# Kernel optimization log

Measured on AMD Instinct MI355X. Metric: run time of the kernel, lower is better.

The kernel has to match this reference:

```python
import jax, jax.numpy as jnp
import numpy as np

T, B, D, H = 1024, 8, 1024, 16

def setup_inputs() -> dict:
    key = jax.random.key(0)
    ks = jax.random.split(key, 9)
    s = 0.02
    return {
        "x": jax.random.normal(ks[0], (T, B, D), dtype=jnp.float32),
        "Wq": jax.random.normal(ks[1], (D, D), dtype=jnp.float32) * s,
        "bq": jnp.zeros((D,), dtype=jnp.float32),
        "Wk": jax.random.normal(ks[2], (D, D), dtype=jnp.float32) * s,
        "bk": jnp.zeros((D,), dtype=jnp.float32),
        "Wv": jax.random.normal(ks[3], (D, D), dtype=jnp.float32) * s,
        "bv": jnp.zeros((D,), dtype=jnp.float32),
        "Wo": jax.random.normal(ks[4], (D, D), dtype=jnp.float32) * s,
        "bo": jnp.zeros((D,), dtype=jnp.float32),
        "n_heads": H,
    }

def reference(x, Wq, bq, Wk, bk, Wv, bv, Wo, bo, n_heads):
    t, b, D = x.shape
    h = n_heads
    d = D // h
    scale = 1.0 / jnp.sqrt(jnp.float32(d))
    # nn.Linear: y = x @ W.T + b
    q = (x @ Wq.T + bq).reshape(t, b, h, d)
    k = (x @ Wk.T + bk).reshape(t, b, h, d)
    v = (x @ Wv.T + bv).reshape(t, b, h, d)
    # scores: [b, h, t_query, t_key]
    scores = jnp.einsum('tbhd,sbhd->bhts', q, k) * scale
    attn = jax.nn.softmax(scores, axis=-1)
    out = jnp.einsum('bhts,sbhd->tbhd', attn, v).reshape(t, b, D)
    return out @ Wo.T + bo
```

## Files before the change

### kernel.cpp

```cpp
#include <hip/hip_runtime.h>


#define Tn 1024
#define Bn 8
#define Dn 1024
#define Hn 16
#define HDn 64
#define Mn 8192
#define Kn 1024

typedef float f32x4 __attribute__((ext_vector_type(4)));
typedef __bf16 bf16x8 __attribute__((ext_vector_type(8)));
typedef unsigned short u16x8 __attribute__((ext_vector_type(8)));
typedef unsigned short u16x4 __attribute__((ext_vector_type(4)));

#define GLL16(g, l)                                                        \
  __builtin_amdgcn_global_load_lds(                                        \
      (const __attribute__((address_space(1))) void*)(g),                  \
      (__attribute__((address_space(3))) void*)(l), 16, 0, 0)

__device__ __forceinline__ unsigned short f2bf(float f) {
  unsigned int u = __float_as_uint(f);
  u += 0x7fffu + ((u >> 16) & 1u);
  return (unsigned short)(u >> 16);
}

__device__ __forceinline__ unsigned short bfbits(float f) {
  __bf16 h = (__bf16)f;
  return __builtin_bit_cast(unsigned short, h);
}

__global__ __launch_bounds__(256) void cvt_all(
    const float* __restrict__ x, const float* __restrict__ w0,
    const float* __restrict__ w1, const float* __restrict__ w2,
    const float* __restrict__ w3, unsigned short* __restrict__ dx,
    unsigned short* __restrict__ d0, unsigned short* __restrict__ d1,
    unsigned short* __restrict__ d2, unsigned short* __restrict__ d3) {
  const int NX = Mn * Kn / 4;
  const int NW = Dn * Dn / 4;
  const int NT = NX + 4 * NW;
  int i = blockIdx.x * 256 + threadIdx.x;
  const int stride = gridDim.x * 256;
  for (; i < NT; i += stride) {
    const float* src;
    unsigned short* dst;
    int j;
    if (i < NX) {
      src = x; dst = dx; j = i;
    } else {
      const int t = i - NX;
      const int wsel = t >> 18;
      j = t & (NW - 1);
      src = (wsel == 0) ? w0 : (wsel == 1) ? w1 : (wsel == 2) ? w2 : w3;
      dst = (wsel == 0) ? d0 : (wsel == 1) ? d1 : (wsel == 2) ? d2 : d3;
    }
    const float4 v = ((const float4*)src)[j];
    u16x4 o;
    o.x = f2bf(v.x); o.y = f2bf(v.y); o.z = f2bf(v.z); o.w = f2bf(v.w);
    ((u16x4*)dst)[j] = o;
  }
}

__device__ __forceinline__ void gemm128_core(
    const unsigned short* __restrict__ A, const unsigned short* __restrict__ Bw,
    unsigned short* lds_a, unsigned short* lds_b,
    int bm, int bn, f32x4 acc[4][4]) {
  const int tid = threadIdx.x;
  const int lane = tid & 63;
  const int w = tid >> 6;
  const int wr = w >> 1, wc = w & 1;
  const int fr = lane & 15, fg = lane >> 4;

  int goffA[4], goffB[4];
#pragma unroll
  for (int i = 0; i < 4; i++) {
    const int p = tid + 256 * i;
    const int r = p >> 3, cblk = (p & 7) ^ (r & 7);
    goffA[i] = (bm * 128 + r) * Kn + cblk * 8;
    goffB[i] = (bn * 128 + r) * Kn + cblk * 8;
  }
  int aoff[4][2], boff[4][2];
#pragma unroll
  for (int m = 0; m < 4; m++) {
    const int row = wr * 64 + m * 16 + fr;
#pragma unroll
    for (int kk = 0; kk < 2; kk++)
      aoff[m][kk] = row * 64 + (((kk * 4 + fg) ^ (row & 7)) * 8);
  }
#pragma unroll
  for (int n = 0; n < 4; n++) {
    const int row = wc * 64 + n * 16 + fr;
#pragma unroll
    for (int kk = 0; kk < 2; kk++)
      boff[n][kk] = row * 64 + (((kk * 4 + fg) ^ (row & 7)) * 8);
  }

  for (int kt = 0; kt < 16; ++kt) {
    const int kbase = kt * 64;
#pragma unroll
    for (int i = 0; i < 4; i++) {
      GLL16(A + goffA[i] + kbase, &lds_a[(tid + 256 * i) * 8]);
      GLL16(Bw + goffB[i] + kbase, &lds_b[(tid + 256 * i) * 8]);
    }
    __syncthreads();
#pragma unroll
    for (int kk = 0; kk < 2; kk++) {
      bf16x8 af[4], bfr[4];
#pragma unroll
      for (int m = 0; m < 4; m++) af[m] = *(const bf16x8*)&lds_a[aoff[m][kk]];
#pragma unroll
      for (int n = 0; n < 4; n++) bfr[n] = *(const bf16x8*)&lds_b[boff[n][kk]];
#pragma unroll
      for (int m = 0; m < 4; m++)
#pragma unroll
        for (int n = 0; n < 4; n++)
          acc[m][n] = __builtin_amdgcn_mfma_f32_16x16x32_bf16(
              af[m], bfr[n], acc[m][n], 0, 0, 0);
    }
    __syncthreads();
  }
}

__global__ __launch_bounds__(256) void gemm_qkv(
    const unsigned short* __restrict__ xbf, const unsigned short* __restrict__ wq,
    const unsigned short* __restrict__ wk, const unsigned short* __restrict__ wv,
    const float* __restrict__ bq, const float* __restrict__ bk,
    const float* __restrict__ bv, unsigned short* __restrict__ qd,
    unsigned short* __restrict__ kd, unsigned short* __restrict__ vd) {
  __shared__ __align__(16) unsigned short lds_a[128 * 64];
  __shared__ __align__(16) unsigned short lds_b[128 * 64];
  const int z = blockIdx.z;
  const unsigned short* Bw = (z == 0) ? wq : (z == 1) ? wk : wv;
  const float* bias = (z == 0) ? bq : (z == 1) ? bk : bv;
  unsigned short* dst = (z == 0) ? qd : (z == 1) ? kd : vd;
  const float sc = (z == 0) ? 0.125f * 1.44269504088896f : 1.0f;

  f32x4 acc[4][4] = {};
  gemm128_core(xbf, Bw, lds_a, lds_b, blockIdx.x, blockIdx.y, acc);

  const int tid = threadIdx.x, lane = tid & 63, w = tid >> 6;
  const int wr = w >> 1, wc = w & 1, fr = lane & 15, fg = lane >> 4;
#pragma unroll
  for (int n = 0; n < 4; n++) {
    const int gcol = blockIdx.y * 128 + wc * 64 + n * 16 + fr;
    const float bc = bias[gcol];
    const int hh = gcol >> 6, dd = gcol & 63;
#pragma unroll
    for (int m = 0; m < 4; m++) {
      const int rowbase = blockIdx.x * 128 + wr * 64 + m * 16 + fg * 4;
#pragma unroll
      for (int r = 0; r < 4; r++) {
        const int grow = rowbase + r;
        const int tt = grow >> 3, bb = grow & 7;
        const float v = (acc[m][n][r] + bc) * sc;
        dst[((size_t)(bb * Hn + hh) * Tn + tt) * HDn + dd] = f2bf(v);
      }
    }
  }
}

__global__ __launch_bounds__(256) void gemm_out(
    const unsigned short* __restrict__ abf, const unsigned short* __restrict__ wo,
    const float* __restrict__ bo, float* __restrict__ out) {
  __shared__ __align__(16) unsigned short lds_a[128 * 64];
  __shared__ __align__(16) unsigned short lds_b[128 * 64];
  f32x4 acc[4][4] = {};
  gemm128_core(abf, wo, lds_a, lds_b, blockIdx.x, blockIdx.y, acc);

  const int tid = threadIdx.x, lane = tid & 63, w = tid >> 6;
  const int wr = w >> 1, wc = w & 1, fr = lane & 15, fg = lane >> 4;
#pragma unroll
  for (int n = 0; n < 4; n++) {
    const int gcol = blockIdx.y * 128 + wc * 64 + n * 16 + fr;
    const float bc = bo[gcol];
#pragma unroll
    for (int m = 0; m < 4; m++) {
      const int rowbase = blockIdx.x * 128 + wr * 64 + m * 16 + fg * 4;
#pragma unroll
      for (int r = 0; r < 4; r++) {
        const int grow = rowbase + r;
        out[(size_t)grow * Dn + gcol] = acc[m][n][r] + bc;
      }
    }
  }
}

__global__ __launch_bounds__(256) void transpose_v(
    const unsigned short* __restrict__ src, unsigned short* __restrict__ dst) {
  __shared__ unsigned short tile[64][72];
  const int tid = threadIdx.x;
  const size_t base = (size_t)blockIdx.y * ((size_t)Tn * HDn);
  const int t0 = blockIdx.x * 64;
#pragma unroll
  for (int it = 0; it < 2; it++) {
    const int p = it * 256 + tid;
    const int r = p >> 3, c = (p & 7) * 8;
    *(u16x8*)&tile[r][c] =
        *(const u16x8*)(src + base + (size_t)(t0 + r) * HDn + c);
  }
  __syncthreads();
#pragma unroll
  for (int it = 0; it < 2; it++) {
    const int p = it * 256 + tid;
    const int d = p >> 3, tc = (p & 7) * 8;
    u16x8 v;
#pragma unroll
    for (int j = 0; j < 8; j++) v[j] = tile[tc + j][d];
    *(u16x8*)(dst + base + (size_t)d * Tn + t0 + tc) = v;
  }
}

__global__ __launch_bounds__(256) void attn_fwd(
    const unsigned short* __restrict__ Q, const unsigned short* __restrict__ K,
    const unsigned short* __restrict__ Vt, unsigned short* __restrict__ Ob) {
  __shared__ __align__(16) unsigned short k2[2][64 * 64];
  __shared__ __align__(16) unsigned short v2[2][64 * 64];
  __shared__ __align__(16) unsigned short p_all[64 * 64];

  const int tid = threadIdx.x, lane = tid & 63, w = tid >> 6;
  const int fr = lane & 15, fg = lane >> 4;
  const int bh = blockIdx.x;
  const int qt = blockIdx.y;
  const int bb = bh >> 4, hh = bh & 15;

  const unsigned short* Qbh = Q + (size_t)bh * (Tn * HDn);
  const unsigned short* Kbh = K + (size_t)bh * (Tn * HDn);
  const unsigned short* Vbh = Vt + (size_t)bh * (HDn * Tn);

  const int p0 = tid, p1 = tid + 256;
  const int r0 = p0 >> 3, c0 = (p0 & 7) ^ (r0 & 7);
  const int r1 = p1 >> 3, c1 = (p1 & 7) ^ (r1 & 7);

  GLL16(Qbh + (size_t)(qt * 64 + r0) * HDn + c0 * 8, &p_all[p0 * 8]);
  GLL16(Qbh + (size_t)(qt * 64 + r1) * HDn + c1 * 8, &p_all[p1 * 8]);
  __syncthreads();
  bf16x8 qa[2];
#pragma unroll
  for (int ks = 0; ks < 2; ks++) {
    const int row = w * 16 + fr;
    const int blk = (ks * 4 + fg) ^ (row & 7);
    qa[ks] = *(const bf16x8*)&p_all[row * 64 + blk * 8];
  }

  bf16x8 vones;
#pragma unroll
  for (int j = 0; j < 8; j++) vones[j] = (__bf16)1.0f;

#define STAGE_KV(nx, bi)                                                     \
  do {                                                                       \
    GLL16(Kbh + (size_t)((nx) * 64 + r0) * HDn + c0 * 8, &k2[bi][p0 * 8]);   \
    GLL16(Kbh + (size_t)((nx) * 64 + r1) * HDn + c1 * 8, &k2[bi][p1 * 8]);   \
    GLL16(Vbh + (size_t)r0 * Tn + (nx) * 64 + c0 * 8, &v2[bi][p0 * 8]);      \
    GLL16(Vbh + (size_t)r1 * Tn + (nx) * 64 + c1 * 8, &v2[bi][p1 * 8]);      \
  } while (0)

  STAGE_KV(0, 0);
  __syncthreads();

  f32x4 o[4] = {};
  float lsum[4] = {};
  const float FM = 12.0f;

  for (int kt = 0; kt < 16; kt++) {
    const int cur = kt & 1;
    if (kt < 15) STAGE_KV(kt + 1, cur ^ 1);
    const unsigned short* kl = k2[cur];
    const unsigned short* vl = v2[cur];

    f32x4 s[4] = {};
    __builtin_amdgcn_s_setprio(1);
#pragma unroll
    for (int n = 0; n < 4; n++)
#pragma unroll
      for (int ks = 0; ks < 2; ks++) {
        const int krow = n * 16 + fr;
        const int blk = (ks * 4 + fg) ^ (krow & 7);
        const bf16x8 kb = *(const bf16x8*)&kl[krow * 64 + blk * 8];
        s[n] = __builtin_amdgcn_mfma_f32_16x16x32_bf16(kb, qa[ks], s[n], 0, 0, 0);
      }
    __builtin_amdgcn_s_setprio(0);

#pragma unroll
    for (int n = 0; n < 4; n++) {
      u16x4 pk;
#pragma unroll
      for (int r = 0; r < 4; r++) pk[r] = bfbits(exp2f(s[n][r] - FM));
      const int addr = (w * 16 + fr) * 64 +
                       (((2 * n + (fg >> 1)) ^ (fr & 7)) * 8) + (fg & 1) * 4;
      *(u16x4*)&p_all[addr] = pk;
    }

    bf16x8 pa[2];
#pragma unroll
    for (int ks = 0; ks < 2; ks++) {
      const int blk = (ks * 4 + fg) ^ (fr & 7);
      pa[ks] = *(const bf16x8*)&p_all[(w * 16 + fr) * 64 + blk * 8];
    }

    f32x4 ss = {};
    ss = __builtin_amdgcn_mfma_f32_16x16x32_bf16(pa[0], vones, ss, 0, 0, 0);
    ss = __builtin_amdgcn_mfma_f32_16x16x32_bf16(pa[1], vones, ss, 0, 0, 0);
#pragma unroll
    for (int r = 0; r < 4; r++) lsum[r] += ss[r];

    __builtin_amdgcn_s_setprio(1);
#pragma unroll
    for (int ks = 0; ks < 2; ks++)
#pragma unroll
      for (int n = 0; n < 4; n++) {
        const int vrow = n * 16 + fr;
        const int vblk = (ks * 4 + fg) ^ (vrow & 7);
        const bf16x8 vb = *(const bf16x8*)&vl[vrow * 64 + vblk * 8];
        o[n] = __builtin_amdgcn_mfma_f32_16x16x32_bf16(pa[ks], vb, o[n], 0, 0, 0);
      }
    __builtin_amdgcn_s_setprio(0);
    __syncthreads();
  }
#undef STAGE_KV

#pragma unroll
  for (int r = 0; r < 4; r++) lsum[r] = 1.0f / lsum[r];
  const int tbase = qt * 64 + w * 16 + fg * 4;
#pragma unroll
  for (int n = 0; n < 4; n++) {
    const int dcol = n * 16 + fr;
#pragma unroll
    for (int r = 0; r < 4; r++) {
      const int tt = tbase + r;
      const float val = o[n][r] * lsum[r];
      Ob[((size_t)(tt * Bn + bb)) * Dn + hh * HDn + dcol] = bfbits(val);
    }
  }
}

extern "C" void kernel_launch(void* const* d_in, const int* in_sizes, int n_in,
                              void* d_out, int out_size, void* d_ws,
                              size_t ws_size, hipStream_t stream) {
  (void)in_sizes; (void)n_in; (void)out_size; (void)ws_size;
  const float* x  = (const float*)d_in[0];
  const float* Wq = (const float*)d_in[1];
  const float* bq = (const float*)d_in[2];
  const float* Wk = (const float*)d_in[3];
  const float* bk = (const float*)d_in[4];
  const float* Wv = (const float*)d_in[5];
  const float* bv = (const float*)d_in[6];
  const float* Wo = (const float*)d_in[7];
  const float* bo = (const float*)d_in[8];
  float* out = (float*)d_out;

  unsigned short* ws  = (unsigned short*)d_ws;
  unsigned short* xbf = ws;
  unsigned short* wqb = xbf + (size_t)Mn * Kn;
  unsigned short* wkb = wqb + (size_t)Dn * Dn;
  unsigned short* wvb = wkb + (size_t)Dn * Dn;
  unsigned short* wob = wvb + (size_t)Dn * Dn;
  unsigned short* qb  = wob + (size_t)Dn * Dn;
  unsigned short* kb  = qb + (size_t)Mn * Dn;
  unsigned short* vb  = kb + (size_t)Mn * Dn;
  unsigned short* vtb = xbf;
  unsigned short* ab  = vb;

  cvt_all<<<2048, 256, 0, stream>>>(
      x, Wq, Wk, Wv, Wo, xbf, wqb, wkb, wvb, wob);

  gemm_qkv<<<dim3(Mn / 128, Dn / 128, 3), 256, 0, stream>>>(
      xbf, wqb, wkb, wvb, bq, bk, bv, qb, kb, vb);
  transpose_v<<<dim3(Tn / 64, Bn * Hn), 256, 0, stream>>>(vb, vtb);
  attn_fwd<<<dim3(Bn * Hn, Tn / 64), 256, 0, stream>>>(qb, kb, vtb, ab);
  gemm_out<<<dim3(Mn / 128, Dn / 128), 256, 0, stream>>>(ab, wob, bo, out);
}
```

Before: 268.1 us.

## Fuse V transpose into QKV GEMM epilogue and vectorize stores via swapped MFMA operands

```diff
diff --git a/kernel.cpp b/kernel.cpp
--- a/kernel.cpp
+++ b/kernel.cpp
@@ -115,7 +115,7 @@
 #pragma unroll
         for (int n = 0; n < 4; n++)
           acc[m][n] = __builtin_amdgcn_mfma_f32_16x16x32_bf16(
-              af[m], bfr[n], acc[m][n], 0, 0, 0);
+              bfr[n], af[m], acc[m][n], 0, 0, 0);
     }
     __syncthreads();
   }
@@ -126,13 +126,12 @@
     const unsigned short* __restrict__ wk, const unsigned short* __restrict__ wv,
     const float* __restrict__ bq, const float* __restrict__ bk,
     const float* __restrict__ bv, unsigned short* __restrict__ qd,
-    unsigned short* __restrict__ kd, unsigned short* __restrict__ vd) {
+    unsigned short* __restrict__ kd, unsigned short* __restrict__ vtd) {
   __shared__ __align__(16) unsigned short lds_a[128 * 64];
   __shared__ __align__(16) unsigned short lds_b[128 * 64];
   const int z = blockIdx.z;
   const unsigned short* Bw = (z == 0) ? wq : (z == 1) ? wk : wv;
   const float* bias = (z == 0) ? bq : (z == 1) ? bk : bv;
-  unsigned short* dst = (z == 0) ? qd : (z == 1) ? kd : vd;
   const float sc = (z == 0) ? 0.125f * 1.44269504088896f : 1.0f;
 
   f32x4 acc[4][4] = {};
@@ -142,18 +141,25 @@
   const int wr = w >> 1, wc = w & 1, fr = lane & 15, fg = lane >> 4;
 #pragma unroll
   for (int n = 0; n < 4; n++) {
-    const int gcol = blockIdx.y * 128 + wc * 64 + n * 16 + fr;
-    const float bc = bias[gcol];
-    const int hh = gcol >> 6, dd = gcol & 63;
+    const int gbase = blockIdx.y * 128 + wc * 64 + n * 16 + fg * 4;
+    const float4 bc4 = *(const float4*)&bias[gbase];
+    const int hh = gbase >> 6, dd0 = gbase & 63;
 #pragma unroll
     for (int m = 0; m < 4; m++) {
-      const int rowbase = blockIdx.x * 128 + wr * 64 + m * 16 + fg * 4;
-#pragma unroll
-      for (int r = 0; r < 4; r++) {
-        const int grow = rowbase + r;
-        const int tt = grow >> 3, bb = grow & 7;
-        const float v = (acc[m][n][r] + bc) * sc;
-        dst[((size_t)(bb * Hn + hh) * Tn + tt) * HDn + dd] = f2bf(v);
+      const int grow = blockIdx.x * 128 + wr * 64 + m * 16 + fr;
+      const int tt = grow >> 3, bb = grow & 7;
+      if (z == 2) {
+#pragma unroll
+        for (int r = 0; r < 4; r++)
+          vtd[((size_t)((bb * Hn + hh) * HDn + dd0 + r)) * Tn + tt] =
+              f2bf(acc[m][n][r] + bc4[r]);
+      } else {
+        unsigned short* dst = (z == 0) ? qd : kd;
+        u16x4 pk;
+#pragma unroll
+        for (int r = 0; r < 4; r++)
+          pk[r] = f2bf((acc[m][n][r] + bc4[r]) * sc);
+        *(u16x4*)&dst[((size_t)(bb * Hn + hh) * Tn + tt) * HDn + dd0] = pk;
       }
     }
   }
@@ -171,42 +177,16 @@
   const int wr = w >> 1, wc = w & 1, fr = lane & 15, fg = lane >> 4;
 #pragma unroll
   for (int n = 0; n < 4; n++) {
-    const int gcol = blockIdx.y * 128 + wc * 64 + n * 16 + fr;
-    const float bc = bo[gcol];
+    const int gbase = blockIdx.y * 128 + wc * 64 + n * 16 + fg * 4;
+    const float4 bc4 = *(const float4*)&bo[gbase];
 #pragma unroll
     for (int m = 0; m < 4; m++) {
-      const int rowbase = blockIdx.x * 128 + wr * 64 + m * 16 + fg * 4;
-#pragma unroll
-      for (int r = 0; r < 4; r++) {
-        const int grow = rowbase + r;
-        out[(size_t)grow * Dn + gcol] = acc[m][n][r] + bc;
-      }
-    }
-  }
-}
-
-__global__ __launch_bounds__(256) void transpose_v(
-    const unsigned short* __restrict__ src, unsigned short* __restrict__ dst) {
-  __shared__ unsigned short tile[64][72];
-  const int tid = threadIdx.x;
-  const size_t base = (size_t)blockIdx.y * ((size_t)Tn * HDn);
-  const int t0 = blockIdx.x * 64;
-#pragma unroll
-  for (int it = 0; it < 2; it++) {
-    const int p = it * 256 + tid;
-    const int r = p >> 3, c = (p & 7) * 8;
-    *(u16x8*)&tile[r][c] =
-        *(const u16x8*)(src + base + (size_t)(t0 + r) * HDn + c);
-  }
-  __syncthreads();
-#pragma unroll
-  for (int it = 0; it < 2; it++) {
-    const int p = it * 256 + tid;
-    const int d = p >> 3, tc = (p & 7) * 8;
-    u16x8 v;
-#pragma unroll
-    for (int j = 0; j < 8; j++) v[j] = tile[tc + j][d];
-    *(u16x8*)(dst + base + (size_t)d * Tn + t0 + tc) = v;
+      const int grow = blockIdx.x * 128 + wr * 64 + m * 16 + fr;
+      float4 val;
+#pragma unroll
+      for (int r = 0; r < 4; r++) val[r] = acc[m][n][r] + bc4[r];
+      *(float4*)&out[(size_t)grow * Dn + gbase] = val;
+    }
   }
 }
 
@@ -356,16 +336,14 @@
   unsigned short* wob = wvb + (size_t)Dn * Dn;
   unsigned short* qb  = wob + (size_t)Dn * Dn;
   unsigned short* kb  = qb + (size_t)Mn * Dn;
-  unsigned short* vb  = kb + (size_t)Mn * Dn;
-  unsigned short* vtb = xbf;
-  unsigned short* ab  = vb;
+  unsigned short* vtb = kb + (size_t)Mn * Dn;
+  unsigned short* ab  = xbf;
 
   cvt_all<<<2048, 256, 0, stream>>>(
       x, Wq, Wk, Wv, Wo, xbf, wqb, wkb, wvb, wob);
 
   gemm_qkv<<<dim3(Mn / 128, Dn / 128, 3), 256, 0, stream>>>(
-      xbf, wqb, wkb, wvb, bq, bk, bv, qb, kb, vb);
-  transpose_v<<<dim3(Tn / 64, Bn * Hn), 256, 0, stream>>>(vb, vtb);
+      xbf, wqb, wkb, wvb, bq, bk, bv, qb, kb, vtb);
   attn_fwd<<<dim3(Bn * Hn, Tn / 64), 256, 0, stream>>>(qb, kb, vtb, ab);
   gemm_out<<<dim3(Mn / 128, Dn / 128), 256, 0, stream>>>(ab, wob, bo, out);
 }
```

Result: slower. 280.1 us (+4.5%).
